# Optimization experiments

Hardware: AMD Instinct MI355X
Metric: run time of the kernel (lower is better)

Reference implementation:

```python
import jax, jax.numpy as jnp
import numpy as np

B, S, E = 2, 2048, 1024
H, D = 16, 64          # num_heads, head_dim
FF = 4096              # ff_dim = 4*E
EPS = 1e-5


def _layer_norm(x, g, b):
    mu = jnp.mean(x, axis=-1, keepdims=True)
    var = jnp.mean(jnp.square(x - mu), axis=-1, keepdims=True)
    return (x - mu) * jax.lax.rsqrt(var + EPS) * g + b


def setup_inputs() -> dict:
    key = jax.random.key(0)
    ks = jax.random.split(key, 9)
    s = lambda fan_in: 1.0 / np.sqrt(fan_in)
    return {
        "x": jax.random.normal(ks[0], (B, S, E), dtype=jnp.float32),
        "w_qkv": jax.random.uniform(ks[1], (3 * E, E), jnp.float32, -s(E), s(E)),
        "b_qkv": jnp.zeros((3 * E,), jnp.float32),
        "w_out": jax.random.uniform(ks[2], (E, E), jnp.float32, -s(E), s(E)),
        "b_out": jnp.zeros((E,), jnp.float32),
        "g1": jnp.ones((E,), jnp.float32),
        "beta1": jnp.zeros((E,), jnp.float32),
        "w_fc1": jax.random.uniform(ks[3], (FF, E), jnp.float32, -s(E), s(E)),
        "b_fc1": jnp.zeros((FF,), jnp.float32),
        "w_fc2": jax.random.uniform(ks[4], (E, FF), jnp.float32, -s(FF), s(FF)),
        "b_fc2": jnp.zeros((E,), jnp.float32),
        "g2": jnp.ones((E,), jnp.float32),
        "beta2": jnp.zeros((E,), jnp.float32),
    }


def reference(x, w_qkv, b_qkv, w_out, b_out, g1, beta1, w_fc1, b_fc1, w_fc2, b_fc2, g2, beta2):
    scale = 1.0 / np.sqrt(D)
    # QKV projection: [B,S,3E] -> [3,B,H,S,D]
    qkv = (x @ w_qkv.T + b_qkv).reshape(B, S, 3, H, D).transpose(2, 0, 3, 1, 4)
    q, k, v = qkv[0], qkv[1], qkv[2]
    attn = jax.nn.softmax(jnp.einsum('bhqd,bhkd->bhqk', q, k) * scale, axis=-1)
    out = jnp.einsum('bhqk,bhkd->bhqd', attn, v)          # [B,H,S,D]
    out = out.transpose(0, 2, 1, 3).reshape(B, S, E)
    attn_out = out @ w_out.T + b_out
    x1 = _layer_norm(x + attn_out, g1, beta1)
    h = jax.nn.gelu(x1 @ w_fc1.T + b_fc1, approximate=False)  # torch GELU = exact erf
    ff_out = h @ w_fc2.T + b_fc2
    return _layer_norm(x1 + ff_out, g2, beta2)
```

## Files before the change

kernel.cpp:

```cpp
#include <hip/hip_runtime.h>
#include <hip/hip_bf16.h>
#include <math.h>
#include <type_traits>

typedef __hip_bfloat16 bf16;
using short8  = __attribute__((ext_vector_type(8))) short;
using short4v = __attribute__((ext_vector_type(4))) short;
using f32x4   = __attribute__((ext_vector_type(4))) float;

#define TS 2048
#define TH 16
#define TD 64
#define TE 1024
#define T3E 3072

__device__ __forceinline__ void gload16(void* lds, const void* g) {
    __builtin_amdgcn_global_load_lds(
        (__attribute__((address_space(1))) void*)g,
        (__attribute__((address_space(3))) void*)lds, 16, 0, 0);
}

__device__ __forceinline__ uint32_t pktrunc(float a, float b) {
    return (__builtin_bit_cast(uint32_t, a) >> 16) |
           (__builtin_bit_cast(uint32_t, b) & 0xFFFF0000u);
}

__global__ __launch_bounds__(256) void f2b_multi(
    const float* __restrict__ s0, bf16* __restrict__ d0,
    const float* __restrict__ s1, bf16* __restrict__ d1,
    const float* __restrict__ s2, bf16* __restrict__ d2,
    const float* __restrict__ s3, bf16* __restrict__ d3,
    const float* __restrict__ s4, bf16* __restrict__ d4)
{
    int blk = blockIdx.x;
    const float* s; bf16* d; int base;
    if (blk < 2048)      { s = s0; d = d0; base = 0; }
    else if (blk < 3584) { s = s1; d = d1; base = 2048; }
    else if (blk < 4096) { s = s2; d = d2; base = 3584; }
    else if (blk < 6144) { s = s3; d = d3; base = 4096; }
    else                 { s = s4; d = d4; base = 6144; }
    size_t i = ((size_t)(blk - base) * 256 + threadIdx.x) * 8;
    float4 a = *(const float4*)&s[i];
    float4 b = *(const float4*)&s[i + 4];
    bf16 t[8];
    t[0] = __float2bfloat16(a.x); t[1] = __float2bfloat16(a.y);
    t[2] = __float2bfloat16(a.z); t[3] = __float2bfloat16(a.w);
    t[4] = __float2bfloat16(b.x); t[5] = __float2bfloat16(b.y);
    t[6] = __float2bfloat16(b.z); t[7] = __float2bfloat16(b.w);
    *(uint4*)&d[i] = *(uint4*)t;
}

template <typename TC, bool GELU, bool QS, bool WVT>
__global__ __launch_bounds__(256) void gemm_bt(
    const bf16* __restrict__ A, const bf16* __restrict__ Bw,
    const float* __restrict__ bias, TC* __restrict__ C,
    bf16* __restrict__ vTout, int M, int N, int K, int kLen)
{
    __shared__ bf16 As[128 * 32];
    __shared__ bf16 Bs[128 * 32];

    const int t    = threadIdx.x;
    const int lane = t & 63;
    const int wave = t >> 6;
    const int wr   = wave >> 1;
    const int wc   = wave & 1;
    const int lr   = lane & 15;
    const int lq   = lane >> 4;
    const int mBase = blockIdx.y * 128;
    const int nBase = blockIdx.x * 128;
    const int kOff  = blockIdx.z * kLen;

    const int srow = lane >> 2;
    const int skc  = (lane & 3) * 8;

    f32x4 acc[4][4];
    #pragma unroll
    for (int mi = 0; mi < 4; mi++)
        #pragma unroll
        for (int ni = 0; ni < 4; ni++)
            acc[mi][ni] = (f32x4){0.f, 0.f, 0.f, 0.f};

    for (int k0 = kOff; k0 < kOff + kLen; k0 += 32) {
        #pragma unroll
        for (int c = 0; c < 2; c++) {
            int r0 = wave * 32 + c * 16;
            gload16(&As[r0 * 32],
                    &A[(size_t)(mBase + r0 + srow) * K + k0 + skc]);
            gload16(&Bs[r0 * 32],
                    &Bw[(size_t)(nBase + r0 + srow) * K + k0 + skc]);
        }
        __syncthreads();

        short8 af[4], bfr[4];
        #pragma unroll
        for (int mi = 0; mi < 4; mi++)
            af[mi] = *(const short8*)&As[(wr * 64 + mi * 16 + lr) * 32 + lq * 8];
        #pragma unroll
        for (int ni = 0; ni < 4; ni++)
            bfr[ni] = *(const short8*)&Bs[(wc * 64 + ni * 16 + lr) * 32 + lq * 8];

        #pragma unroll
        for (int mi = 0; mi < 4; mi++)
            #pragma unroll
            for (int ni = 0; ni < 4; ni++)
                acc[mi][ni] = __builtin_amdgcn_mfma_f32_16x16x32_bf16(
                    af[mi], bfr[ni], acc[mi][ni], 0, 0, 0);
        __syncthreads();
    }

    const size_t cOff = (size_t)blockIdx.z * M * N;
    #pragma unroll
    for (int mi = 0; mi < 4; mi++) {
        #pragma unroll
        for (int ni = 0; ni < 4; ni++) {
            int cc = nBase + wc * 64 + ni * 16 + lr;
            float bv = (blockIdx.z == 0) ? bias[cc] : 0.f;
            int r0 = mBase + wr * 64 + mi * 16 + lq * 4;
            bool vpath = false;
            if constexpr (WVT) {
                if (cc >= 2 * TE) {
                    vpath = true;
                    int d  = cc - 2 * TE;
                    int s0 = r0 & (TS - 1);
                    int bb = r0 >> 11;
                    int pos = (s0 & ~31) | (((s0 >> 2) & 3) << 3)
                            | (((s0 >> 4) & 1) << 2);
                    bf16 ob[4];
                    #pragma unroll
                    for (int i = 0; i < 4; i++)
                        ob[i] = __float2bfloat16(acc[mi][ni][i] + bv);
                    *(uint2*)&vTout[((size_t)(bb * TH + (d >> 6)) * TD + (d & 63))
                                    * TS + pos] = *(uint2*)ob;
                }
            }
            if (!vpath) {
                #pragma unroll
                for (int i = 0; i < 4; i++) {
                    float v = acc[mi][ni][i] + bv;
                    if constexpr (GELU)
                        v = 0.5f * v * (1.0f + erff(v * 0.70710678118f));
                    if constexpr (QS)
                        if (cc < TE) v *= 0.180336880111f;
                    if constexpr (std::is_same_v<TC, bf16>)
                        C[cOff + (size_t)(r0 + i) * N + cc] = __float2bfloat16(v);
                    else
                        C[cOff + (size_t)(r0 + i) * N + cc] = v;
                }
            }
        }
    }
}

__global__ __launch_bounds__(256, 4) void attn_flash(
    const bf16* __restrict__ qkv, const bf16* __restrict__ vT,
    bf16* __restrict__ attnO)
{
    __shared__ bf16 Ks[128 * 72];
    __shared__ bf16 Vt[64 * 136];

    const int t    = threadIdx.x;
    const int lane = t & 63;
    const int wv   = t >> 6;
    const int c    = lane & 15;
    const int u    = lane >> 4;
    const int bid  = blockIdx.x;
    const int bh   = (bid & 7) * 4 + ((bid >> 3) & 3);
    const int qt   = bid >> 5;
    const int h = bh & 15, b = bh >> 4;
    const size_t tokBase = (size_t)b * TS;
    const int qrow = qt * 64 + wv * 16 + c;

    short8 qf[2];
    #pragma unroll
    for (int kc = 0; kc < 2; kc++)
        qf[kc] = *(const short8*)&qkv[(tokBase + qrow) * T3E + h * TD + kc * 32 + u * 8];

    f32x4 oacc[4];
    #pragma unroll
    for (int di = 0; di < 4; di++) oacc[di] = (f32x4){0.f, 0.f, 0.f, 0.f};
    float lsum = 0.f;

    const int vd = t >> 2;
    const int vc = (t & 3) * 8;
    const bf16* vbase = &vT[((size_t)bh * TD + vd) * TS + vc];

    for (int it = 0; it < 16; it++) {
        const int kb0 = it * 128;
        __syncthreads();

        #pragma unroll
        for (int i = 0; i < 4; i++) {
            int l = t + i * 256;
            int r = l >> 3, ch = (l & 7) * 8;
            *(uint4*)&Ks[r * 72 + ch] =
                *(const uint4*)&qkv[(tokBase + kb0 + r) * T3E + TE + h * TD + ch];
        }
        #pragma unroll
        for (int i = 0; i < 4; i++)
            *(uint4*)&Vt[vd * 136 + vc + i * 32] = *(const uint4*)&vbase[kb0 + i * 32];
        __syncthreads();

        f32x4 sacc[8];
        #pragma unroll
        for (int kc = 0; kc < 2; kc++) {
            #pragma unroll
            for (int kb = 0; kb < 8; kb++) {
                short8 kf = *(const short8*)&Ks[(kb * 16 + c) * 72 + kc * 32 + u * 8];
                sacc[kb] = __builtin_amdgcn_mfma_f32_16x16x32_bf16(
                    kf, qf[kc],
                    kc == 0 ? (f32x4){0.f, 0.f, 0.f, 0.f} : sacc[kb], 0, 0, 0);
            }
        }

        #pragma unroll
        for (int p = 0; p < 4; p++) {
            union { uint32_t d[2]; short4v s; } pb0, pb1;
            {
                float a0 = exp2f(sacc[2*p][0]);
                float a1 = exp2f(sacc[2*p][1]);
                float a2 = exp2f(sacc[2*p][2]);
                float a3 = exp2f(sacc[2*p][3]);
                float b0 = exp2f(sacc[2*p+1][0]);
                float b1 = exp2f(sacc[2*p+1][1]);
                float b2 = exp2f(sacc[2*p+1][2]);
                float b3 = exp2f(sacc[2*p+1][3]);
                lsum += (a0 + a1) + (a2 + a3) + (b0 + b1) + (b2 + b3);
                pb0.d[0] = pktrunc(a0, a1); pb0.d[1] = pktrunc(a2, a3);
                pb1.d[0] = pktrunc(b0, b1); pb1.d[1] = pktrunc(b2, b3);
            }
            #pragma unroll
            for (int di = 0; di < 4; di++) {
                short8 vv = *(const short8*)&Vt[(di * 16 + c) * 136 + p * 32 + u * 8];
                short4v lo = __builtin_shufflevector(vv, vv, 0, 1, 2, 3);
                short4v hi = __builtin_shufflevector(vv, vv, 4, 5, 6, 7);
                oacc[di] = __builtin_amdgcn_mfma_f32_16x16x16bf16_1k(
                    lo, pb0.s, oacc[di], 0, 0, 0);
                oacc[di] = __builtin_amdgcn_mfma_f32_16x16x16bf16_1k(
                    hi, pb1.s, oacc[di], 0, 0, 0);
            }
        }
    }

    lsum += __shfl_xor(lsum, 16, 64);
    lsum += __shfl_xor(lsum, 32, 64);
    const float inv = 1.0f / lsum;

    #pragma unroll
    for (int di = 0; di < 4; di++) {
        bf16 ob[4];
        #pragma unroll
        for (int rg = 0; rg < 4; rg++)
            ob[rg] = __float2bfloat16(oacc[di][rg] * inv);
        *(uint2*)&attnO[(tokBase + qrow) * TE + h * TD + di * 16 + u * 4] = *(uint2*)ob;
    }
}

__global__ __launch_bounds__(256) void add_ln3(
    const float* __restrict__ a, const float* __restrict__ p0,
    const float* __restrict__ p1, const float* __restrict__ g,
    const float* __restrict__ beta, float* __restrict__ out,
    bf16* __restrict__ outb)
{
    __shared__ float r1[256], r2[256];
    const int t = threadIdx.x;
    const size_t row = (size_t)blockIdx.x * TE;

    float4 va = *(const float4*)&a[row + t * 4];
    float4 v0 = *(const float4*)&p0[row + t * 4];
    float4 v1 = *(const float4*)&p1[row + t * 4];
    float v[4] = {va.x + v0.x + v1.x, va.y + v0.y + v1.y,
                  va.z + v0.z + v1.z, va.w + v0.w + v1.w};
    float s = 0.f, s2 = 0.f;
    #pragma unroll
    for (int i = 0; i < 4; i++) { s += v[i]; s2 += v[i] * v[i]; }
    r1[t] = s; r2[t] = s2;
    __syncthreads();
    for (int off = 128; off > 0; off >>= 1) {
        if (t < off) { r1[t] += r1[t + off]; r2[t] += r2[t + off]; }
        __syncthreads();
    }
    const float mu  = r1[0] * (1.f / 1024.f);
    const float var = r2[0] * (1.f / 1024.f) - mu * mu;
    const float rs  = rsqrtf(var + 1e-5f);
    float4 vg  = *(const float4*)&g[t * 4];
    float4 vbt = *(const float4*)&beta[t * 4];
    float o[4];
    o[0] = (v[0] - mu) * rs * vg.x + vbt.x;
    o[1] = (v[1] - mu) * rs * vg.y + vbt.y;
    o[2] = (v[2] - mu) * rs * vg.z + vbt.z;
    o[3] = (v[3] - mu) * rs * vg.w + vbt.w;
    *(float4*)&out[row + t * 4] = *(float4*)o;
    if (outb) {
        bf16 ob[4];
        #pragma unroll
        for (int i = 0; i < 4; i++) ob[i] = __float2bfloat16(o[i]);
        *(uint2*)&outb[row + t * 4] = *(uint2*)ob;
    }
}

extern "C" void kernel_launch(void* const* d_in, const int* in_sizes, int n_in,
                              void* d_out, int out_size, void* d_ws, size_t ws_size,
                              hipStream_t stream)
{
    const float* x     = (const float*)d_in[0];
    const float* w_qkv = (const float*)d_in[1];
    const float* b_qkv = (const float*)d_in[2];
    const float* w_out = (const float*)d_in[3];
    const float* b_out = (const float*)d_in[4];
    const float* g1    = (const float*)d_in[5];
    const float* beta1 = (const float*)d_in[6];
    const float* w_fc1 = (const float*)d_in[7];
    const float* b_fc1 = (const float*)d_in[8];
    const float* w_fc2 = (const float*)d_in[9];
    const float* b_fc2 = (const float*)d_in[10];
    const float* g2    = (const float*)d_in[11];
    const float* beta2 = (const float*)d_in[12];
    float* out = (float*)d_out;

    char* wsb   = (char*)d_ws;
    bf16*  qkv   = (bf16*)(wsb);
    bf16*  hbuf  = (bf16*)(wsb);
    bf16*  attnO = (bf16*)(wsb + 33554432);
    bf16*  vT    = (bf16*)(wsb + 41943040);
    float* y     = (float*)(wsb + 41943040);
    float* ff    = y;
    bf16*  xb    = (bf16*)(wsb + 75497472);
    float* x1    = (float*)(wsb + 75497472);
    bf16*  x1b   = (bf16*)(wsb + 92274688);
    bf16*  wqkvb = (bf16*)(wsb + 100663296);
    bf16*  woutb = (bf16*)(wsb + 106954752);
    bf16*  wfc1b = (bf16*)(wsb + 109051904);
    bf16*  wfc2b = (bf16*)(wsb + 117440512);

    const int M = 2 * TS;
    const size_t PART = (size_t)M * TE;
    dim3 blk(256);

    f2b_multi<<<dim3(8192), blk, 0, stream>>>(
        x, xb, w_qkv, wqkvb, w_out, woutb, w_fc1, wfc1b, w_fc2, wfc2b);

    gemm_bt<bf16, false, true, true><<<dim3(24, 32, 1), blk, 0, stream>>>(
        xb, wqkvb, b_qkv, qkv, vT, M, T3E, TE, TE);
    attn_flash<<<dim3(1024), blk, 0, stream>>>(qkv, vT, attnO);
    gemm_bt<float, false, false, false><<<dim3(8, 32, 2), blk, 0, stream>>>(
        attnO, woutb, b_out, y, nullptr, M, TE, TE, TE / 2);
    add_ln3<<<dim3(M), blk, 0, stream>>>(x, y, y + PART, g1, beta1, x1, x1b);
    gemm_bt<bf16, true, false, false><<<dim3(32, 32, 1), blk, 0, stream>>>(
        x1b, wfc1b, b_fc1, hbuf, nullptr, M, 4096, TE, TE);
    gemm_bt<float, false, false, false><<<dim3(8, 32, 2), blk, 0, stream>>>(
        hbuf, wfc2b, b_fc2, ff, nullptr, M, TE, 4096, 2048);
    add_ln3<<<dim3(M), blk, 0, stream>>>(x1, ff, ff + PART, g2, beta2, out, nullptr);
}
```

Before: 406.4 us.

## Replace 128x128 GEMM with double-buffered 256-row tiles and XCD-aware block remap

Replaces the GEMM kernel with a 512-thread version using 256xBN tiles (BN 256 or 128), a K-step of 64, and double-buffered LDS filled by async global-to-LDS loads. Explicit vmcnt waits let the next tile load while the current one is computed. Block IDs are remapped in an interleaved pattern across the XCDs. QK output now uses a 2E row stride because V goes only to the transposed buffer, and the workspace layout is reshuffled. The larger tiles raise per-block data reuse and cut per-step sync overhead, at the cost of much higher LDS and register use, lower occupancy, and fewer blocks per GEMM.

After: 411.2 us. No clear change (+1.2%).

```diff
diff --git a/kernel.cpp b/kernel.cpp
--- a/kernel.cpp
+++ b/kernel.cpp
@@ -12,7 +12,7 @@
 #define TH 16
 #define TD 64
 #define TE 1024
-#define T3E 3072
+#define T2E 2048
 
 __device__ __forceinline__ void gload16(void* lds, const void* g) {
     __builtin_amdgcn_global_load_lds(
@@ -50,72 +50,110 @@
     *(uint4*)&d[i] = *(uint4*)t;
 }
 
-template <typename TC, bool GELU, bool QS, bool WVT>
-__global__ __launch_bounds__(256) void gemm_bt(
+template <typename TC, bool GELU, bool QS, bool WVT, int BN>
+__global__ __launch_bounds__(512, 2) void gemm256(
     const bf16* __restrict__ A, const bf16* __restrict__ Bw,
     const float* __restrict__ bias, TC* __restrict__ C,
-    bf16* __restrict__ vTout, int M, int N, int K, int kLen)
-{
-    __shared__ bf16 As[128 * 32];
-    __shared__ bf16 Bs[128 * 32];
+    bf16* __restrict__ vTout, int M, int N, int K, int kLen, int Cstride)
+{
+    constexpr int NB = BN / 64;
+    constexpr int NI = BN / 64;
+    constexpr int WN = BN / 4;
+    __shared__ bf16 As[2][256 * 64];
+    __shared__ bf16 Bs[2][BN * 64];
 
     const int t    = threadIdx.x;
     const int lane = t & 63;
-    const int wave = t >> 6;
-    const int wr   = wave >> 1;
-    const int wc   = wave & 1;
+    const int wv   = t >> 6;
+    const int wr   = wv >> 2;
+    const int wc   = wv & 3;
     const int lr   = lane & 15;
     const int lq   = lane >> 4;
-    const int mBase = blockIdx.y * 128;
-    const int nBase = blockIdx.x * 128;
-    const int kOff  = blockIdx.z * kLen;
-
-    const int srow = lane >> 2;
-    const int skc  = (lane & 3) * 8;
-
-    f32x4 acc[4][4];
-    #pragma unroll
-    for (int mi = 0; mi < 4; mi++)
-        #pragma unroll
-        for (int ni = 0; ni < 4; ni++)
+
+    const int gx  = gridDim.x, gxy = gridDim.x * gridDim.y;
+    const int nwg = gxy * gridDim.z;
+    const int id  = blockIdx.x + gx * blockIdx.y + gxy * blockIdx.z;
+    const int sid = (id & 7) * (nwg >> 3) + (id >> 3);
+    const int zIdx  = sid / gxy;
+    const int rem   = sid - zIdx * gxy;
+    const int tm    = rem / gx;
+    const int mBase = tm * 256;
+    const int nBase = (rem - tm * gx) * BN;
+    const int kOff  = zIdx * kLen;
+
+    const int sr = t >> 3;
+    const int sc = (t & 7) * 8;
+    const int NT = kLen >> 6;
+
+    const bf16* aPt = A  + (size_t)(mBase + sr) * K + sc;
+    const bf16* bPt = Bw + (size_t)(nBase + sr) * K + sc;
+
+    f32x4 acc[8][NI];
+    #pragma unroll
+    for (int mi = 0; mi < 8; mi++)
+        #pragma unroll
+        for (int ni = 0; ni < NI; ni++)
             acc[mi][ni] = (f32x4){0.f, 0.f, 0.f, 0.f};
 
-    for (int k0 = kOff; k0 < kOff + kLen; k0 += 32) {
-        #pragma unroll
-        for (int c = 0; c < 2; c++) {
-            int r0 = wave * 32 + c * 16;
-            gload16(&As[r0 * 32],
-                    &A[(size_t)(mBase + r0 + srow) * K + k0 + skc]);
-            gload16(&Bs[r0 * 32],
-                    &Bw[(size_t)(nBase + r0 + srow) * K + k0 + skc]);
-        }
-        __syncthreads();
-
-        short8 af[4], bfr[4];
-        #pragma unroll
-        for (int mi = 0; mi < 4; mi++)
-            af[mi] = *(const short8*)&As[(wr * 64 + mi * 16 + lr) * 32 + lq * 8];
-        #pragma unroll
-        for (int ni = 0; ni < 4; ni++)
-            bfr[ni] = *(const short8*)&Bs[(wc * 64 + ni * 16 + lr) * 32 + lq * 8];
-
-        #pragma unroll
-        for (int mi = 0; mi < 4; mi++)
+    auto stage = [&](int b, int k0) {
+        #pragma unroll
+        for (int i = 0; i < 4; i++)
+            gload16(&As[b][i * 4096 + wv * 512],
+                    aPt + (size_t)(i * 64) * K + k0);
+        #pragma unroll
+        for (int i = 0; i < NB; i++)
+            gload16(&Bs[b][i * 4096 + wv * 512],
+                    bPt + (size_t)(i * 64) * K + k0);
+    };
+
+    stage(0, kOff);
+    for (int kt = 0; kt < NT; ++kt) {
+        const int cur = kt & 1;
+        if (kt + 1 < NT) {
+            stage(cur ^ 1, kOff + (kt + 1) * 64);
+            if constexpr (BN == 256)
+                asm volatile("s_waitcnt vmcnt(8)" ::: "memory");
+            else
+                asm volatile("s_waitcnt vmcnt(6)" ::: "memory");
+        } else {
+            asm volatile("s_waitcnt vmcnt(0)" ::: "memory");
+        }
+        __builtin_amdgcn_s_barrier();
+        asm volatile("" ::: "memory");
+
+        short8 bfr[NI][2];
+        #pragma unroll
+        for (int ni = 0; ni < NI; ni++)
             #pragma unroll
-            for (int ni = 0; ni < 4; ni++)
+            for (int ks = 0; ks < 2; ks++)
+                bfr[ni][ks] = *(const short8*)
+                    &Bs[cur][(wc * WN + ni * 16 + lr) * 64 + ks * 32 + lq * 8];
+        #pragma unroll
+        for (int mi = 0; mi < 8; mi++) {
+            short8 a0 = *(const short8*)
+                &As[cur][(wr * 128 + mi * 16 + lr) * 64 + lq * 8];
+            short8 a1 = *(const short8*)
+                &As[cur][(wr * 128 + mi * 16 + lr) * 64 + 32 + lq * 8];
+            #pragma unroll
+            for (int ni = 0; ni < NI; ni++) {
                 acc[mi][ni] = __builtin_amdgcn_mfma_f32_16x16x32_bf16(
-                    af[mi], bfr[ni], acc[mi][ni], 0, 0, 0);
-        __syncthreads();
-    }
-
-    const size_t cOff = (size_t)blockIdx.z * M * N;
-    #pragma unroll
-    for (int mi = 0; mi < 4; mi++) {
-        #pragma unroll
-        for (int ni = 0; ni < 4; ni++) {
-            int cc = nBase + wc * 64 + ni * 16 + lr;
-            float bv = (blockIdx.z == 0) ? bias[cc] : 0.f;
-            int r0 = mBase + wr * 64 + mi * 16 + lq * 4;
+                    a0, bfr[ni][0], acc[mi][ni], 0, 0, 0);
+                acc[mi][ni] = __builtin_amdgcn_mfma_f32_16x16x32_bf16(
+                    a1, bfr[ni][1], acc[mi][ni], 0, 0, 0);
+            }
+        }
+        asm volatile("" ::: "memory");
+        __builtin_amdgcn_s_barrier();
+    }
+
+    const size_t cOff = (size_t)zIdx * M * Cstride;
+    #pragma unroll
+    for (int mi = 0; mi < 8; mi++) {
+        #pragma unroll
+        for (int ni = 0; ni < NI; ni++) {
+            int cc = nBase + wc * WN + ni * 16 + lr;
+            float bv = (zIdx == 0) ? bias[cc] : 0.f;
+            int r0 = mBase + wr * 128 + mi * 16 + lq * 4;
             bool vpath = false;
             if constexpr (WVT) {
                 if (cc >= 2 * TE) {
@@ -142,9 +180,9 @@
                     if constexpr (QS)
                         if (cc < TE) v *= 0.180336880111f;
                     if constexpr (std::is_same_v<TC, bf16>)
-                        C[cOff + (size_t)(r0 + i) * N + cc] = __float2bfloat16(v);
+                        C[cOff + (size_t)(r0 + i) * Cstride + cc] = __float2bfloat16(v);
                     else
-                        C[cOff + (size_t)(r0 + i) * N + cc] = v;
+                        C[cOff + (size_t)(r0 + i) * Cstride + cc] = v;
                 }
             }
         }
@@ -173,7 +211,7 @@
     short8 qf[2];
     #pragma unroll
     for (int kc = 0; kc < 2; kc++)
-        qf[kc] = *(const short8*)&qkv[(tokBase + qrow) * T3E + h * TD + kc * 32 + u * 8];
+        qf[kc] = *(const short8*)&qkv[(tokBase + qrow) * T2E + h * TD + kc * 32 + u * 8];
 
     f32x4 oacc[4];
     #pragma unroll
@@ -193,7 +231,7 @@
             int l = t + i * 256;
             int r = l >> 3, ch = (l & 7) * 8;
             *(uint4*)&Ks[r * 72 + ch] =
-                *(const uint4*)&qkv[(tokBase + kb0 + r) * T3E + TE + h * TD + ch];
+                *(const uint4*)&qkv[(tokBase + kb0 + r) * T2E + TE + h * TD + ch];
         }
         #pragma unroll
         for (int i = 0; i < 4; i++)
@@ -318,36 +356,36 @@
     float* out = (float*)d_out;
 
     char* wsb   = (char*)d_ws;
-    bf16*  qkv   = (bf16*)(wsb);
-    bf16*  hbuf  = (bf16*)(wsb);
+    bf16*  qk    = (bf16*)(wsb);
+    bf16*  vT    = (bf16*)(wsb + 16777216);
+    bf16*  xb    = (bf16*)(wsb + 25165824);
+    float* y     = (float*)(wsb);
+    float* ff    = (float*)(wsb);
     bf16*  attnO = (bf16*)(wsb + 33554432);
-    bf16*  vT    = (bf16*)(wsb + 41943040);
-    float* y     = (float*)(wsb + 41943040);
-    float* ff    = y;
-    bf16*  xb    = (bf16*)(wsb + 75497472);
-    float* x1    = (float*)(wsb + 75497472);
-    bf16*  x1b   = (bf16*)(wsb + 92274688);
-    bf16*  wqkvb = (bf16*)(wsb + 100663296);
-    bf16*  woutb = (bf16*)(wsb + 106954752);
-    bf16*  wfc1b = (bf16*)(wsb + 109051904);
+    bf16*  x1b   = (bf16*)(wsb + 33554432);
+    bf16*  wfc1b = (bf16*)(wsb + 41943040);
+    bf16*  woutb = (bf16*)(wsb + 50331648);
+    bf16*  wqkvb = (bf16*)(wsb + 52428800);
+    float* x1    = (float*)(wsb + 67108864);
+    bf16*  hbuf  = (bf16*)(wsb + 83886080);
     bf16*  wfc2b = (bf16*)(wsb + 117440512);
 
     const int M = 2 * TS;
     const size_t PART = (size_t)M * TE;
-    dim3 blk(256);
+    dim3 blk(256), blk5(512);
 
     f2b_multi<<<dim3(8192), blk, 0, stream>>>(
         x, xb, w_qkv, wqkvb, w_out, woutb, w_fc1, wfc1b, w_fc2, wfc2b);
 
-    gemm_bt<bf16, false, true, true><<<dim3(24, 32, 1), blk, 0, stream>>>(
-        xb, wqkvb, b_qkv, qkv, vT, M, T3E, TE, TE);
-    attn_flash<<<dim3(1024), blk, 0, stream>>>(qkv, vT, attnO);
-    gemm_bt<float, false, false, false><<<dim3(8, 32, 2), blk, 0, stream>>>(
-        attnO, woutb, b_out, y, nullptr, M, TE, TE, TE / 2);
+    gemm256<bf16, false, true, true, 256><<<dim3(12, 16, 1), blk5, 0, stream>>>(
+        xb, wqkvb, b_qkv, qk, vT, M, 3072, TE, TE, T2E);
+    attn_flash<<<dim3(1024), blk, 0, stream>>>(qk, vT, attnO);
+    gemm256<float, false, false, false, 128><<<dim3(8, 16, 2), blk5, 0, stream>>>(
+        attnO, woutb, b_out, y, nullptr, M, TE, TE, TE / 2, TE);
     add_ln3<<<dim3(M), blk, 0, stream>>>(x, y, y + PART, g1, beta1, x1, x1b);
-    gemm_bt<bf16, true, false, false><<<dim3(32, 32, 1), blk, 0, stream>>>(
-        x1b, wfc1b, b_fc1, hbuf, nullptr, M, 4096, TE, TE);
-    gemm_bt<float, false, false, false><<<dim3(8, 32, 2), blk, 0, stream>>>(
-        hbuf, wfc2b, b_fc2, ff, nullptr, M, TE, 4096, 2048);
+    gemm256<bf16, true, false, false, 256><<<dim3(16, 16, 1), blk5, 0, stream>>>(
+        x1b, wfc1b, b_fc1, hbuf, nullptr, M, 4096, TE, TE, 4096);
+    gemm256<float, false, false, false, 128><<<dim3(8, 16, 2), blk5, 0, stream>>>(
+        hbuf, wfc2b, b_fc2, ff, nullptr, M, TE, 4096, 2048, TE);
     add_ln3<<<dim3(M), blk, 0, stream>>>(x1, ff, ff + PART, g2, beta2, out, nullptr);
 }
```
